# Optimization experiments

Measured on AMD Instinct MI355X. Metric: run time of the kernel, lower is better.

## Reference

```python
import jax, jax.numpy as jnp
import numpy as np


def setup_inputs() -> dict:
    key = jax.random.key(0)
    ks = jax.random.split(key, 8)
    B, N, K, C_in, M, C_add, C_out = 2, 40000, 16, 64, 16, 3, 128
    in_features = (C_in + C_add) * M  # 1072
    input_features = jax.random.normal(ks[0], (B, N, C_in), dtype=jnp.float32)
    neighbor_inds = jax.random.randint(ks[1], (B, N, K), 0, N, dtype=jnp.int64)
    inverse_neighbors = jax.random.randint(ks[2], (B, N * K), 0, N * K, dtype=jnp.int64)
    inverse_k = jax.random.randint(ks[3], (B, N * K), 0, K, dtype=jnp.int64)
    inverse_idx = jax.random.randint(ks[4], (B, N * K), 0, N, dtype=jnp.int64)
    weightnet = jax.random.normal(ks[5], (B, N, K, M), dtype=jnp.float32)
    additional_features = jax.random.normal(ks[6], (B, N, K, C_add), dtype=jnp.float32)
    bound = 1.0 / np.sqrt(in_features)
    kw, kb = jax.random.split(ks[7])
    linear_weight = jax.random.uniform(kw, (C_out, in_features), dtype=jnp.float32, minval=-bound, maxval=bound)
    linear_bias = jax.random.uniform(kb, (C_out,), dtype=jnp.float32, minval=-bound, maxval=bound)
    return {
        "input_features": input_features,
        "neighbor_inds": neighbor_inds,
        "inverse_neighbors": inverse_neighbors,
        "inverse_k": inverse_k,
        "inverse_idx": inverse_idx,
        "weightnet": weightnet,
        "additional_features": additional_features,
        "linear_weight": linear_weight,
        "linear_bias": linear_bias,
    }


def reference(input_features, neighbor_inds, inverse_neighbors, inverse_k, inverse_idx,
              weightnet, additional_features, linear_weight, linear_bias):
    # inverse_* tensors are only used by the custom CUDA backward; unused here.
    B, N, K = neighbor_inds.shape
    # gather neighbor features: [B, N, K, C_in]
    gathered = jnp.take_along_axis(input_features[:, :, None, :],
                                   neighbor_inds[..., None], axis=1)
    # concat extra per-neighbor features -> [B, N, K, C]
    feats = jnp.concatenate([gathered, additional_features], axis=-1)
    # PConv: [B,N,C,K] @ [B,N,K,M] -> [B,N,C,M] -> flatten to [B,N,C*M]
    pconv = jnp.einsum('bnkc,bnkm->bncm', feats, weightnet)
    pconv = pconv.reshape(B, N, -1)
    # fused linear
    out = jnp.einsum('bnf,of->bno', pconv, linear_weight) + linear_bias
    return out
```

## Files before the change

kernel.cpp:

```cpp
#include <hip/hip_runtime.h>
#include <stdint.h>

typedef unsigned short u16;
typedef short short8 __attribute__((ext_vector_type(8)));
typedef float floatx4 __attribute__((ext_vector_type(4)));

#define NPERB   40000
#define NPTS    80000
#define KNBR    16
#define CIN     64
#define MDIM    16
#define CADD    3
#define CF      (CIN + CADD)
#define COUT    128
#define KF      1072
#define KP      1088
#define NKT     34
#define PTSB    16
#define SLAB    65
#define GR      64
#define PPB     8

__device__ __forceinline__ u16 f2bf(float f) {
    union { float f; unsigned int u; } v; v.f = f;
    unsigned int u = v.u;
    return (u16)((u + 0x7FFFu + ((u >> 16) & 1u)) >> 16);
}
__device__ __forceinline__ short8 pack8(floatx4 x, floatx4 y) {
    union { short8 v; u16 a[8]; } u;
    u.a[0] = f2bf(x[0]); u.a[1] = f2bf(x[1]); u.a[2] = f2bf(x[2]); u.a[3] = f2bf(x[3]);
    u.a[4] = f2bf(y[0]); u.a[5] = f2bf(y[1]); u.a[6] = f2bf(y[2]); u.a[7] = f2bf(y[3]);
    return u.v;
}
__device__ __forceinline__ unsigned swz(unsigned chunk) {
    return chunk ^ ((chunk >> 3) & 7u);
}
__device__ __forceinline__ unsigned aswz(unsigned c) {
    return c ^ ((c >> 4) & 3u);
}
__device__ __forceinline__ void gload_lds16(const void* g, void* l) {
    __builtin_amdgcn_global_load_lds(
        (const __attribute__((address_space(1))) void*)g,
        (__attribute__((address_space(3))) void*)l, 16, 0, 0);
}

__global__ void prep_lw_kernel(const float* __restrict__ lw, u16* __restrict__ lwp) {
    int i = blockIdx.x * 256 + threadIdx.x;
    if (i >= COUT * KP) return;
    int o = i / KP, f = i - o * KP;
    lwp[i] = (f < KF) ? f2bf(lw[(size_t)o * KF + f]) : (u16)0;
}

__device__ __forceinline__ void emit_point(
    int lane, float av, const float (&fv)[KNBR], const float* wl,
    u16* __restrict__ dst)
{
    const int em = lane & 15, ec = lane >> 4;
    float ev = 0.f;
#pragma unroll
    for (int k = 0; k < KNBR; k++)
        ev += __shfl(av, k * CADD + ec) * wl[k * MDIM + em];
    if (ec == 3) ev = 0.f;
    dst[1024 + lane] = f2bf(ev);

    floatx4 a0 = 0, a1 = 0, a2 = 0, a3 = 0;
#pragma unroll
    for (int k = 0; k < KNBR; k++) {
        const floatx4* w4 = (const floatx4*)(wl + k * MDIM);
        const float fvk = fv[k];
        a0 += fvk * w4[0]; a1 += fvk * w4[1];
        a2 += fvk * w4[2]; a3 += fvk * w4[3];
    }
    *(short8*)(dst + lane * 16)     = pack8(a0, a1);
    *(short8*)(dst + lane * 16 + 8) = pack8(a2, a3);
}

__global__ __launch_bounds__(256) void pconv_kernel(
    const float* __restrict__ inp,
    const int*   __restrict__ nbr,
    const float* __restrict__ wn,
    const float* __restrict__ addl,
    u16* __restrict__ pc)
{
    __shared__ __align__(16) float Wns[PPB * KNBR * MDIM];

    const int wave = threadIdx.x >> 6;
    const int lane = threadIdx.x & 63;
    const int pbase = blockIdx.x * PPB;
    const float* inpb = inp + ((pbase >= NPERB) ? (size_t)NPERB * CIN : 0);

    const int pr0 = wave * 2;
    const int p0  = __builtin_amdgcn_readfirstlane(pbase + pr0);
    const int p1  = p0 + 1;

    float* wl0 = Wns + pr0 * (KNBR * MDIM);
    float* wl1 = wl0 + KNBR * MDIM;
    gload_lds16(wn + (size_t)p0 * (KNBR * MDIM) + lane * 4, wl0);
    gload_lds16(wn + (size_t)p1 * (KNBR * MDIM) + lane * 4, wl1);

    float av0 = (lane < KNBR * CADD) ? addl[(size_t)p0 * (KNBR * CADD) + lane] : 0.f;
    float av1 = (lane < KNBR * CADD) ? addl[(size_t)p1 * (KNBR * CADD) + lane] : 0.f;

    const int* nb0 = nbr + (size_t)p0 * KNBR;
    const int* nb1 = nbr + (size_t)p1 * KNBR;
    int idx0[KNBR], idx1[KNBR];
#pragma unroll
    for (int k = 0; k < KNBR; k++) idx0[k] = nb0[k];
#pragma unroll
    for (int k = 0; k < KNBR; k++) idx1[k] = nb1[k];

    float fv0[KNBR], fv1[KNBR];
#pragma unroll
    for (int k = 0; k < KNBR; k++) fv0[k] = inpb[(size_t)idx0[k] * CIN + lane];
#pragma unroll
    for (int k = 0; k < KNBR; k++) fv1[k] = inpb[(size_t)idx1[k] * CIN + lane];

    asm volatile("s_waitcnt vmcnt(0)" ::: "memory");
    __builtin_amdgcn_sched_barrier(0);

    emit_point(lane, av0, fv0, wl0, pc + (size_t)p0 * KP);
    emit_point(lane, av1, fv1, wl1, pc + (size_t)p1 * KP);
}

__global__ __launch_bounds__(512) void gemm_kernel(
    const u16* __restrict__ pc,
    const u16* __restrict__ lwp,
    const float* __restrict__ bias,
    float* __restrict__ out)
{
    __shared__ __align__(16) u16 At[2][GR * 32];

    const int wave = threadIdx.x >> 6;
    const int lane = threadIdx.x & 63;
    const int pbase = blockIdx.x * GR;
    const int r16 = lane & 15, quad = lane >> 4;
    const int rt = wave & 3;
    const int c0 = (wave >> 2) * 64;

    const u16* ssrc = nullptr;
    if (wave < 4) {
        unsigned s = (unsigned)wave * 64 + lane;
        unsigned c = aswz(s);
        ssrc = pc + (size_t)(pbase + (c >> 2)) * KP + (c & 3u) * 8;
    }
    u16* sdst0 = &At[0][(size_t)wave * 64 * 8];
    u16* sdst1 = &At[1][(size_t)wave * 64 * 8];

    const unsigned ca = (unsigned)(rt * 16 + r16) * 4 + quad;
    const unsigned slot = aswz(ca);

    const u16* B0 = lwp + (size_t)(c0 + r16) * KP + quad * 8;
    const u16* B1 = B0 + (size_t)16 * KP;
    const u16* B2 = B0 + (size_t)32 * KP;
    const u16* B3 = B0 + (size_t)48 * KP;
    const float bv0 = bias[c0 + r16];
    const float bv1 = bias[c0 + 16 + r16];
    const float bv2 = bias[c0 + 32 + r16];
    const float bv3 = bias[c0 + 48 + r16];

    if (wave < 4) gload_lds16(ssrc, sdst0);
    asm volatile("s_waitcnt vmcnt(0)" ::: "memory");
    __syncthreads();

    floatx4 acc0 = 0, acc1 = 0, acc2 = 0, acc3 = 0;
    int cur = 0;
    for (int kt = 0; kt < NKT; kt++) {
        if (kt + 1 < NKT && wave < 4)
            gload_lds16(ssrc + (size_t)(kt + 1) * 32, cur ? sdst0 : sdst1);

        short8 A  = *(const short8*)&At[cur][slot * 8];
        short8 b0 = *(const short8*)(B0 + kt * 32);
        short8 b1 = *(const short8*)(B1 + kt * 32);
        short8 b2 = *(const short8*)(B2 + kt * 32);
        short8 b3 = *(const short8*)(B3 + kt * 32);
        acc0 = __builtin_amdgcn_mfma_f32_16x16x32_bf16(A, b0, acc0, 0, 0, 0);
        acc1 = __builtin_amdgcn_mfma_f32_16x16x32_bf16(A, b1, acc1, 0, 0, 0);
        acc2 = __builtin_amdgcn_mfma_f32_16x16x32_bf16(A, b2, acc2, 0, 0, 0);
        acc3 = __builtin_amdgcn_mfma_f32_16x16x32_bf16(A, b3, acc3, 0, 0, 0);

        __syncthreads();
        cur ^= 1;
    }

#pragma unroll
    for (int r = 0; r < 4; r++) {
        const size_t row = (size_t)(pbase + rt * 16 + quad * 4 + r) * COUT;
        out[row + c0 + r16]      = acc0[r] + bv0;
        out[row + c0 + 16 + r16] = acc1[r] + bv1;
        out[row + c0 + 32 + r16] = acc2[r] + bv2;
        out[row + c0 + 48 + r16] = acc3[r] + bv3;
    }
}

__device__ __forceinline__ void compute_point(
    int pr, int lane, float av, const float (&fv)[KNBR],
    const float* wl, u16* Apc)
{
    const int em = lane & 15, ec = lane >> 4;
    float ev = 0.f;
#pragma unroll
    for (int k = 0; k < KNBR; k++)
        ev += __shfl(av, k * CADD + ec) * wl[k * MDIM + em];
    if (ec == 3) ev = 0.f;
    {
        unsigned kt   = 32 + (lane >> 5);
        unsigned quad = (lane >> 3) & 3;
        unsigned ch   = kt * SLAB + (unsigned)pr * 4 + quad;
        Apc[swz(ch) * 8 + (lane & 7)] = f2bf(ev);
    }
    floatx4 a0 = 0, a1 = 0, a2 = 0, a3 = 0;
#pragma unroll
    for (int k = 0; k < KNBR; k++) {
        const floatx4* w4 = (const floatx4*)(wl + k * MDIM);
        const float fvk = fv[k];
        a0 += fvk * w4[0]; a1 += fvk * w4[1];
        a2 += fvk * w4[2]; a3 += fvk * w4[3];
    }
    {
        unsigned kt = lane >> 1, qb = (lane & 1) * 2;
        unsigned ch = kt * SLAB + (unsigned)pr * 4 + qb;
        *(short8*)&Apc[swz(ch) * 8]     = pack8(a0, a1);
        *(short8*)&Apc[swz(ch + 1) * 8] = pack8(a2, a3);
    }
}

__global__ __launch_bounds__(512, 6) void fused_kernel(
    const float* __restrict__ inp, const int* __restrict__ nbr,
    const float* __restrict__ wn, const float* __restrict__ addl,
    const u16* __restrict__ lwp, const float* __restrict__ bias,
    float* __restrict__ out)
{
    __shared__ __align__(16) u16   Apc[(NKT * SLAB + 8) * 8];
    __shared__ __align__(16) float Wns[PTSB * KNBR * MDIM];

    const int wave = threadIdx.x >> 6;
    const int lane = threadIdx.x & 63;
    const int pbase = blockIdx.x * PTSB;
    const float* inpb = inp + ((pbase >= NPERB) ? (size_t)NPERB * CIN : 0);

    const int pr0 = wave * 2;
    const int p0  = __builtin_amdgcn_readfirstlane(pbase + pr0);
    const int p1  = p0 + 1;

    float* wl0 = Wns + pr0 * (KNBR * MDIM);
    float* wl1 = wl0 + KNBR * MDIM;
    gload_lds16(wn + (size_t)p0 * (KNBR * MDIM) + lane * 4, wl0);
    gload_lds16(wn + (size_t)p1 * (KNBR * MDIM) + lane * 4, wl1);

    float av0 = (lane < KNBR * CADD) ? addl[(size_t)p0 * (KNBR * CADD) + lane] : 0.f;
    float av1 = (lane < KNBR * CADD) ? addl[(size_t)p1 * (KNBR * CADD) + lane] : 0.f;

    const int* nb0 = nbr + (size_t)p0 * KNBR;
    const int* nb1 = nbr + (size_t)p1 * KNBR;
    int idx0[KNBR], idx1[KNBR];
#pragma unroll
    for (int k = 0; k < KNBR; k++) idx0[k] = nb0[k];
#pragma unroll
    for (int k = 0; k < KNBR; k++) idx1[k] = nb1[k];

    float fv0[KNBR], fv1[KNBR];
#pragma unroll
    for (int k = 0; k < KNBR; k++) fv0[k] = inpb[(size_t)idx0[k] * CIN + lane];
#pragma unroll
    for (int k = 0; k < KNBR; k++) fv1[k] = inpb[(size_t)idx1[k] * CIN + lane];

    asm volatile("s_waitcnt vmcnt(0)" ::: "memory");
    __builtin_amdgcn_sched_barrier(0);

    compute_point(pr0,     lane, av0, fv0, wl0, Apc);
    compute_point(pr0 + 1, lane, av1, fv1, wl1, Apc);

    const int r16 = lane & 15, quad = lane >> 4;
    const int c0 = wave * 16;
    const u16* Bp = lwp + (size_t)(c0 + r16) * KP + quad * 8;
    const unsigned abase = (unsigned)r16 * 4 + quad;
    const float bv = bias[c0 + r16];

    __syncthreads();

    floatx4 acc = 0;
#pragma unroll 2
    for (int kt = 0; kt < NKT; kt++) {
        short8 A = *(const short8*)&Apc[swz((unsigned)kt * SLAB + abase) * 8];
        short8 B = *(const short8*)(Bp + kt * 32);
        acc = __builtin_amdgcn_mfma_f32_16x16x32_bf16(A, B, acc, 0, 0, 0);
    }

#pragma unroll
    for (int r = 0; r < 4; r++) {
        const size_t row = (size_t)(pbase + quad * 4 + r) * COUT;
        out[row + c0 + r16] = acc[r] + bv;
    }
}

__global__ __launch_bounds__(256) void fused_fallback_kernel(
    const float* __restrict__ inp, const int* __restrict__ nbr,
    const float* __restrict__ wn, const float* __restrict__ addl,
    const float* __restrict__ lw, const float* __restrict__ bias,
    float* __restrict__ out)
{
    const int p = blockIdx.x;
    const int b = p / NPERB;
    const int tid = threadIdx.x;
    __shared__ float sf[KNBR * CF];
    __shared__ float sw[KNBR * MDIM];
    __shared__ float sp[KF];

    sw[tid] = wn[(size_t)p * (KNBR * MDIM) + tid];
    for (int i = tid; i < KNBR * CIN; i += 256) {
        int k = i >> 6, c = i & 63;
        int idx = nbr[(size_t)p * KNBR + k];
        sf[k * CF + c] = inp[((size_t)b * NPERB + idx) * CIN + c];
    }
    if (tid < KNBR * CADD) {
        int k = tid / CADD, c = tid - k * CADD;
        sf[k * CF + CIN + c] = addl[(size_t)p * (KNBR * CADD) + tid];
    }
    __syncthreads();
    for (int f = tid; f < KF; f += 256) {
        int c = f >> 4, m = f & 15;
        float s = 0;
#pragma unroll
        for (int k = 0; k < KNBR; k++) s += sf[k * CF + c] * sw[k * MDIM + m];
        sp[f] = s;
    }
    __syncthreads();
    const int o = tid >> 1, h = tid & 1;
    float s = 0;
    for (int f = h * (KF / 2); f < (h + 1) * (KF / 2); f++)
        s += sp[f] * lw[(size_t)o * KF + f];
    s += __shfl_xor(s, 1);
    if (h == 0) out[(size_t)p * COUT + o] = s + bias[o];
}

extern "C" void kernel_launch(void* const* d_in, const int* in_sizes, int n_in,
                              void* d_out, int out_size, void* d_ws, size_t ws_size,
                              hipStream_t stream) {
    const float* inp  = (const float*)d_in[0];
    const int*   nbr  = (const int*)d_in[1];
    const float* wn   = (const float*)d_in[5];
    const float* addl = (const float*)d_in[6];
    const float* lw   = (const float*)d_in[7];
    const float* bias = (const float*)d_in[8];
    float* out = (float*)d_out;

    const size_t lw_bytes = (size_t)COUT * KP * sizeof(u16);
    const size_t pc_bytes = (size_t)NPTS * KP * sizeof(u16);

    if (ws_size >= lw_bytes + pc_bytes) {
        u16* lwp = (u16*)d_ws;
        u16* pcw = lwp + (size_t)COUT * KP;
        prep_lw_kernel<<<(COUT * KP + 255) / 256, 256, 0, stream>>>(lw, lwp);
        pconv_kernel<<<NPTS / PPB, 256, 0, stream>>>(inp, nbr, wn, addl, pcw);
        gemm_kernel<<<NPTS / GR, 512, 0, stream>>>(pcw, lwp, bias, out);
    } else if (ws_size >= lw_bytes) {
        u16* lwp = (u16*)d_ws;
        prep_lw_kernel<<<(COUT * KP + 255) / 256, 256, 0, stream>>>(lw, lwp);
        fused_kernel<<<NPTS / PTSB, 512, 0, stream>>>(inp, nbr, wn, addl, lwp, bias, out);
    } else {
        fused_fallback_kernel<<<NPTS, 256, 0, stream>>>(inp, nbr, wn, addl, lw, bias, out);
    }
}
```

Before: 378.4 us.

## Rewrite GEMM kernel with register-tiled 32x128 per-wave tiles and direct global loads

Replaces the LDS double-buffered GEMM, where each wave computed a 16x64 tile, with a register-only scheme. Each wave now owns 32 rows by all 128 output columns and loads A and B fragments straight from global memory, double-buffered in registers across k-steps. Block size goes from 512 to 256 threads and rows per block from 64 to 128. This drops LDS traffic and the per-k-step barriers and reuses each B fragment across two row tiles, at the cost of much higher register pressure (64 accumulator VGPRs plus buffers) and reliance on cache for B reuse.

After: 343.7 us. -9.2%, faster.

```diff
diff --git a/kernel.cpp b/kernel.cpp
--- a/kernel.cpp
+++ b/kernel.cpp
@@ -18,7 +18,7 @@
 #define NKT     34
 #define PTSB    16
 #define SLAB    65
-#define GR      64
+#define GR      128
 #define PPB     8
 
 __device__ __forceinline__ u16 f2bf(float f) {
@@ -34,9 +34,6 @@
 }
 __device__ __forceinline__ unsigned swz(unsigned chunk) {
     return chunk ^ ((chunk >> 3) & 7u);
-}
-__device__ __forceinline__ unsigned aswz(unsigned c) {
-    return c ^ ((c >> 4) & 3u);
 }
 __device__ __forceinline__ void gload_lds16(const void* g, void* l) {
     __builtin_amdgcn_global_load_lds(
@@ -122,73 +119,68 @@
     emit_point(lane, av1, fv1, wl1, pc + (size_t)p1 * KP);
 }
 
-__global__ __launch_bounds__(512) void gemm_kernel(
+__global__ __launch_bounds__(256) void gemm_kernel(
     const u16* __restrict__ pc,
     const u16* __restrict__ lwp,
     const float* __restrict__ bias,
     float* __restrict__ out)
 {
-    __shared__ __align__(16) u16 At[2][GR * 32];
-
     const int wave = threadIdx.x >> 6;
     const int lane = threadIdx.x & 63;
-    const int pbase = blockIdx.x * GR;
     const int r16 = lane & 15, quad = lane >> 4;
-    const int rt = wave & 3;
-    const int c0 = (wave >> 2) * 64;
-
-    const u16* ssrc = nullptr;
-    if (wave < 4) {
-        unsigned s = (unsigned)wave * 64 + lane;
-        unsigned c = aswz(s);
-        ssrc = pc + (size_t)(pbase + (c >> 2)) * KP + (c & 3u) * 8;
-    }
-    u16* sdst0 = &At[0][(size_t)wave * 64 * 8];
-    u16* sdst1 = &At[1][(size_t)wave * 64 * 8];
-
-    const unsigned ca = (unsigned)(rt * 16 + r16) * 4 + quad;
-    const unsigned slot = aswz(ca);
-
-    const u16* B0 = lwp + (size_t)(c0 + r16) * KP + quad * 8;
-    const u16* B1 = B0 + (size_t)16 * KP;
-    const u16* B2 = B0 + (size_t)32 * KP;
-    const u16* B3 = B0 + (size_t)48 * KP;
-    const float bv0 = bias[c0 + r16];
-    const float bv1 = bias[c0 + 16 + r16];
-    const float bv2 = bias[c0 + 32 + r16];
-    const float bv3 = bias[c0 + 48 + r16];
-
-    if (wave < 4) gload_lds16(ssrc, sdst0);
-    asm volatile("s_waitcnt vmcnt(0)" ::: "memory");
-    __syncthreads();
-
-    floatx4 acc0 = 0, acc1 = 0, acc2 = 0, acc3 = 0;
-    int cur = 0;
-    for (int kt = 0; kt < NKT; kt++) {
-        if (kt + 1 < NKT && wave < 4)
-            gload_lds16(ssrc + (size_t)(kt + 1) * 32, cur ? sdst0 : sdst1);
-
-        short8 A  = *(const short8*)&At[cur][slot * 8];
-        short8 b0 = *(const short8*)(B0 + kt * 32);
-        short8 b1 = *(const short8*)(B1 + kt * 32);
-        short8 b2 = *(const short8*)(B2 + kt * 32);
-        short8 b3 = *(const short8*)(B3 + kt * 32);
-        acc0 = __builtin_amdgcn_mfma_f32_16x16x32_bf16(A, b0, acc0, 0, 0, 0);
-        acc1 = __builtin_amdgcn_mfma_f32_16x16x32_bf16(A, b1, acc1, 0, 0, 0);
-        acc2 = __builtin_amdgcn_mfma_f32_16x16x32_bf16(A, b2, acc2, 0, 0, 0);
-        acc3 = __builtin_amdgcn_mfma_f32_16x16x32_bf16(A, b3, acc3, 0, 0, 0);
-
-        __syncthreads();
-        cur ^= 1;
-    }
-
-#pragma unroll
-    for (int r = 0; r < 4; r++) {
-        const size_t row = (size_t)(pbase + rt * 16 + quad * 4 + r) * COUT;
-        out[row + c0 + r16]      = acc0[r] + bv0;
-        out[row + c0 + 16 + r16] = acc1[r] + bv1;
-        out[row + c0 + 32 + r16] = acc2[r] + bv2;
-        out[row + c0 + 48 + r16] = acc3[r] + bv3;
+    const int row0 = blockIdx.x * GR + wave * 32;
+
+    const u16* pA0 = pc + (size_t)(row0 + r16) * KP + quad * 8;
+    const u16* pA1 = pA0 + (size_t)16 * KP;
+    const u16* pB  = lwp + (size_t)r16 * KP + quad * 8;
+
+    floatx4 acc0[8], acc1[8];
+#pragma unroll
+    for (int n = 0; n < 8; n++) { acc0[n] = 0; acc1[n] = 0; }
+
+    short8 Ac0, Ac1, Bc[8];
+    short8 An0, An1, Bn[8];
+    Ac0 = *(const short8*)pA0;
+    Ac1 = *(const short8*)pA1;
+#pragma unroll
+    for (int n = 0; n < 8; n++)
+        Bc[n] = *(const short8*)(pB + (size_t)n * 16 * KP);
+
+    for (int kt = 0; kt + 1 < NKT; kt += 2) {
+        An0 = *(const short8*)(pA0 + (kt + 1) * 32);
+        An1 = *(const short8*)(pA1 + (kt + 1) * 32);
+#pragma unroll
+        for (int n = 0; n < 8; n++)
+            Bn[n] = *(const short8*)(pB + (size_t)n * 16 * KP + (kt + 1) * 32);
+#pragma unroll
+        for (int n = 0; n < 8; n++) {
+            acc0[n] = __builtin_amdgcn_mfma_f32_16x16x32_bf16(Ac0, Bc[n], acc0[n], 0, 0, 0);
+            acc1[n] = __builtin_amdgcn_mfma_f32_16x16x32_bf16(Ac1, Bc[n], acc1[n], 0, 0, 0);
+        }
+        if (kt + 2 < NKT) {
+            Ac0 = *(const short8*)(pA0 + (kt + 2) * 32);
+            Ac1 = *(const short8*)(pA1 + (kt + 2) * 32);
+#pragma unroll
+            for (int n = 0; n < 8; n++)
+                Bc[n] = *(const short8*)(pB + (size_t)n * 16 * KP + (kt + 2) * 32);
+        }
+#pragma unroll
+        for (int n = 0; n < 8; n++) {
+            acc0[n] = __builtin_amdgcn_mfma_f32_16x16x32_bf16(An0, Bn[n], acc0[n], 0, 0, 0);
+            acc1[n] = __builtin_amdgcn_mfma_f32_16x16x32_bf16(An1, Bn[n], acc1[n], 0, 0, 0);
+        }
+    }
+
+#pragma unroll
+    for (int n = 0; n < 8; n++) {
+        const float bv = bias[n * 16 + r16];
+#pragma unroll
+        for (int r = 0; r < 4; r++) {
+            size_t row = (size_t)(row0 + quad * 4 + r) * COUT;
+            out[row + n * 16 + r16] = acc0[n][r] + bv;
+            row = (size_t)(row0 + 16 + quad * 4 + r) * COUT;
+            out[row + n * 16 + r16] = acc1[n][r] + bv;
+        }
     }
 }
 
@@ -352,7 +344,7 @@
         u16* pcw = lwp + (size_t)COUT * KP;
         prep_lw_kernel<<<(COUT * KP + 255) / 256, 256, 0, stream>>>(lw, lwp);
         pconv_kernel<<<NPTS / PPB, 256, 0, stream>>>(inp, nbr, wn, addl, pcw);
-        gemm_kernel<<<NPTS / GR, 512, 0, stream>>>(pcw, lwp, bias, out);
+        gemm_kernel<<<NPTS / GR, 256, 0, stream>>>(pcw, lwp, bias, out);
     } else if (ws_size >= lw_bytes) {
         u16* lwp = (u16*)d_ws;
         prep_lw_kernel<<<(COUT * KP + 255) / 256, 256, 0, stream>>>(lw, lwp);
```
